# Performance work log

Hardware: AMD Instinct MI355X
Metric: run time of the kernel (lower is better)

Reference implementation:

```python
import jax, jax.numpy as jnp
import numpy as np

B, L, H, T_MAX, D_ID, D_SZ, D_POS = 64, 1024, 256, 128, 128, 64, 128
V_ID, V_SZ = 65536, 256


def setup_inputs() -> dict:
    key = jax.random.key(0)
    ks = jax.random.split(key, 16)
    s = 0.02
    inp = {
        'obj_id': jax.random.randint(ks[0], (B,), 0, V_ID, dtype=jnp.int32),
        'obj_size': jax.random.randint(ks[1], (B,), 0, V_SZ, dtype=jnp.int32),
        'cache_lines': jax.random.randint(ks[2], (B, L), 0, V_ID, dtype=jnp.int32),
        'lengths': jax.random.randint(ks[3], (B,), 0, L, dtype=jnp.int32),
        'c0': jax.random.normal(ks[4], (B, H), jnp.float32),
        'h0': jax.random.normal(ks[5], (B, H), jnp.float32),
        'history': jax.random.normal(ks[6], (B, T_MAX - 1, H), jnp.float32),
        # learned parameters
        'obj_id_table': jax.random.normal(ks[7], (V_ID, D_ID), jnp.float32) * s,
        'obj_size_table': jax.random.normal(ks[8], (V_SZ, D_SZ), jnp.float32) * s,
        'pos_table': jax.random.normal(ks[9], (T_MAX, D_POS), jnp.float32) * s,
        'W_ih': jax.random.normal(ks[10], (4 * H, D_ID + D_SZ), jnp.float32) * s,
        'W_hh': jax.random.normal(ks[11], (4 * H, H), jnp.float32) * s,
        'b_ih': jnp.zeros((4 * H,), jnp.float32),
        'b_hh': jnp.zeros((4 * H,), jnp.float32),
        'attn_W': jax.random.normal(ks[12], (D_ID, H), jnp.float32) * s,
        'scorer_W': jax.random.normal(ks[13], (1, H + D_POS), jnp.float32) * s,
        'scorer_b': jnp.zeros((1,), jnp.float32),
        'reuse_W': jax.random.normal(ks[14], (1, H + D_POS), jnp.float32) * s,
        'reuse_b': jnp.zeros((1,), jnp.float32),
    }
    return inp


def reference(obj_id, obj_size, cache_lines, lengths, c0, h0, history,
              obj_id_table, obj_size_table, pos_table,
              W_ih, W_hh, b_ih, b_hh, attn_W,
              scorer_W, scorer_b, reuse_W, reuse_b):
    # --- embed current access and run one LSTMCell step ---
    x = jnp.concatenate([obj_id_table[obj_id], obj_size_table[obj_size]], axis=-1)  # (B, D_ID+D_SZ)
    gates = x @ W_ih.T + b_ih + h0 @ W_hh.T + b_hh  # (B, 4H)
    i, f, g, o = jnp.split(gates, 4, axis=-1)
    c = jax.nn.sigmoid(f) * c0 + jax.nn.sigmoid(i) * jnp.tanh(g)
    h = jax.nn.sigmoid(o) * jnp.tanh(c)

    # --- growing hidden-state history (deque bounded at max_attention_history) ---
    hist = jnp.concatenate([history, h[:, None, :]], axis=1)  # (B, T, H)
    T = hist.shape[1]
    pos = jnp.broadcast_to(pos_table[:T][None], (hist.shape[0], T, pos_table.shape[1]))
    values = jnp.concatenate([hist, pos], axis=-1)  # (B, T, H+P)

    # --- cache line embeddings (cache_lines_embedder == obj_id_embedder) ---
    q = obj_id_table[cache_lines]  # (B, L, D_ID)

    # --- General (bilinear) multi-query attention over history ---
    scores = jnp.einsum('bld,dh,bth->blt', q, attn_W, hist)  # (B, L, T)
    weights = jax.nn.softmax(scores, axis=-1)
    contexts = jnp.einsum('blt,btv->blv', weights, values)  # (B, L, H+P)

    # --- heads ---
    line_scores = jax.nn.softmax((contexts @ scorer_W.T + scorer_b)[..., 0], axis=-1)  # (B, L)
    pred_reuse = (contexts @ reuse_W.T + reuse_b)[..., 0]  # (B, L)

    # --- mask_renormalize over valid (unpadded) cache lines ---
    valid = jnp.maximum(lengths, 1)[:, None]  # min_len=1 in pad()
    mask = (jnp.arange(line_scores.shape[1])[None, :] < valid).astype(line_scores.dtype)
    masked = line_scores * mask
    denom = masked.sum(axis=-1, keepdims=True)
    probs = masked / jnp.where(denom > 0, denom, 1.0)
    return probs, pred_reuse
```

## Files before the change

kernel.cpp:

```cpp
#include <hip/hip_runtime.h>
#include <math.h>

#define BB 64
#define LL 1024
#define HH 256
#define TT 128
#define D_ID 128
#define D_SZ 64
#define D_POS 128
#define DX 192

typedef short s16x8 __attribute__((ext_vector_type(8)));
typedef float f32x16 __attribute__((ext_vector_type(16)));
typedef unsigned short u16x8 __attribute__((ext_vector_type(8)));

__device__ __forceinline__ unsigned short f2bf(float f) {
    unsigned u = __float_as_uint(f);
    unsigned r = u + 0x7fffu + ((u >> 16) & 1u);
    return (unsigned short)(r >> 16);
}

__device__ __forceinline__ s16x8 pack8(float4 a, float4 b) {
    u16x8 p;
    p[0] = f2bf(a.x); p[1] = f2bf(a.y); p[2] = f2bf(a.z); p[3] = f2bf(a.w);
    p[4] = f2bf(b.x); p[5] = f2bf(b.y); p[6] = f2bf(b.z); p[7] = f2bf(b.w);
    return (s16x8)p;
}

__global__ void embed_kernel(const int* __restrict__ obj_id,
                             const int* __restrict__ obj_size,
                             const float* __restrict__ h0,
                             const float* __restrict__ obj_id_table,
                             const float* __restrict__ obj_size_table,
                             float* __restrict__ xh_t) {
    int tid = threadIdx.x;
    int b = tid & 63;
    int k = blockIdx.x * 4 + (tid >> 6);
    float v;
    if (k < D_ID)      v = obj_id_table[(size_t)obj_id[b] * D_ID + k];
    else if (k < DX)   v = obj_size_table[(size_t)obj_size[b] * D_SZ + (k - D_ID)];
    else               v = h0[b * HH + (k - DX)];
    xh_t[k * 64 + b] = v;
}

__global__ void gates_kernel(const float* __restrict__ xh_t,
                             const float* __restrict__ W_ih,
                             const float* __restrict__ W_hh,
                             const float* __restrict__ b_ih,
                             const float* __restrict__ b_hh,
                             const float* __restrict__ c0,
                             float* __restrict__ h_new) {
    int j = blockIdx.x;
    int tid = threadIdx.x;
    int b = tid & 63;
    int q = __builtin_amdgcn_readfirstlane(tid >> 6);
    int r = q * HH + j;
    __shared__ float gS[256];

    float acc = b_ih[r] + b_hh[r];
    const float* wi = W_ih + (size_t)r * DX;
    const float* wh = W_hh + (size_t)r * HH;
#pragma unroll 16
    for (int k = 0; k < DX; ++k)
        acc += wi[k] * xh_t[k * 64 + b];
#pragma unroll 16
    for (int k = 0; k < HH; ++k)
        acc += wh[k] * xh_t[(DX + k) * 64 + b];
    gS[q * 64 + b] = acc;
    __syncthreads();

    if (tid < 64) {
        float ig = 1.f / (1.f + expf(-gS[tid]));
        float fg = 1.f / (1.f + expf(-gS[64 + tid]));
        float gg = tanhf(gS[128 + tid]);
        float og = 1.f / (1.f + expf(-gS[192 + tid]));
        float c = fg * c0[tid * HH + j] + ig * gg;
        h_new[tid * HH + j] = og * tanhf(c);
    }
}

__global__ void proj_kernel(const float* __restrict__ history,
                            const float* __restrict__ h_new,
                            const float* __restrict__ attn_W,
                            const float* __restrict__ pos_table,
                            const float* __restrict__ scorer_W,
                            const float* __restrict__ reuse_W,
                            unsigned short* __restrict__ hp,
                            float* __restrict__ sv,
                            float* __restrict__ rv) {
    int blk = blockIdx.x;
    int tid = threadIdx.x;

    if (blk >= BB * 16) {
        int idx = blk - BB * 16;
        int b = idx >> 2;
        int which = (idx >> 1) & 1;
        int t = (idx & 1) * 64 + tid;
        const float* w = which ? reuse_W : scorer_W;
        const float* hrow = (t < TT - 1)
            ? history + ((size_t)b * (TT - 1) + t) * HH
            : h_new + (size_t)b * HH;
        float acc = 0.f;
#pragma unroll 8
        for (int k = 0; k < HH / 4; ++k) {
            float4 hv = *(const float4*)(hrow + 4 * k);
            float4 wv = *(const float4*)(w + 4 * k);
            acc += hv.x * wv.x + hv.y * wv.y + hv.z * wv.z + hv.w * wv.w;
        }
        const float* prow = pos_table + (size_t)t * D_POS;
#pragma unroll 8
        for (int k = 0; k < D_POS / 4; ++k) {
            float4 pv = *(const float4*)(prow + 4 * k);
            float4 wv = *(const float4*)(w + HH + 4 * k);
            acc += pv.x * wv.x + pv.y * wv.y + pv.z * wv.z + pv.w * wv.w;
        }
        (which ? rv : sv)[b * TT + t] = acc;
        return;
    }

    int b  = blk >> 4;
    int t0 = ((blk >> 2) & 3) * 32;
    int d0 = (blk & 3) * 32;
    int lane = tid;
    int ln = lane & 31, half = lane >> 5;

    int t = t0 + ln;
    const float* arow = (t < TT - 1)
        ? history + ((size_t)b * (TT - 1) + t) * HH
        : h_new + (size_t)b * HH;
    const float* brow = attn_W + (size_t)(d0 + ln) * HH;

    f32x16 acc;
#pragma unroll
    for (int r = 0; r < 16; ++r) acc[r] = 0.f;

#pragma unroll
    for (int ks = 0; ks < 16; ++ks) {
        int off = ks * 16 + half * 8;
        float4 a0 = *(const float4*)(arow + off);
        float4 a1 = *(const float4*)(arow + off + 4);
        float4 b0 = *(const float4*)(brow + off);
        float4 b1 = *(const float4*)(brow + off + 4);
        acc = __builtin_amdgcn_mfma_f32_32x32x16_bf16(
            pack8(a0, a1), pack8(b0, b1), acc, 0, 0, 0);
    }

#pragma unroll
    for (int r = 0; r < 16; ++r) {
        int tt = t0 + (r & 3) + 8 * (r >> 2) + 4 * half;
        hp[((size_t)b * TT + tt) * D_ID + d0 + ln] = f2bf(acc[r]);
    }
}

__global__ void attn_kernel(const int* __restrict__ cache_lines,
                            const float* __restrict__ obj_id_table,
                            const unsigned short* __restrict__ hp,
                            const float* __restrict__ sv,
                            const float* __restrict__ rv,
                            const float* __restrict__ scorer_b,
                            const float* __restrict__ reuse_b,
                            float* __restrict__ logits,
                            float* __restrict__ out_reuse) {
    int b  = blockIdx.x >> 3;
    int l0 = (blockIdx.x & 7) * 128;
    int tid = threadIdx.x;
    __shared__ unsigned short qS[16384];
    __shared__ unsigned short hpS[16384];

    {
        int l = tid & 127;
        int cl = cache_lines[b * LL + l0 + l];
        const float* qrow = obj_id_table + (size_t)cl * D_ID;
        int lhi = (l >> 5) * 8, llo = l & 31;
#pragma unroll
        for (int i = 0; i < 8; ++i) {
            int u = 2 * i + (tid >> 7);
            float4 f0 = *(const float4*)(qrow + u * 8);
            float4 f1 = *(const float4*)(qrow + u * 8 + 4);
            *(s16x8*)(qS + (((lhi + (u >> 1)) * 64) + (u & 1) * 32 + llo) * 8) =
                pack8(f0, f1);
        }
    }
    {
        int t = tid & 127;
        const unsigned short* hrow = hp + ((size_t)b * TT + t) * D_ID;
        int thi = t >> 5, tlo = t & 31;
#pragma unroll
        for (int i = 0; i < 8; ++i) {
            int u = 2 * i + (tid >> 7);
            u16x8 p = *(const u16x8*)(hrow + u * 8);
            *(u16x8*)(hpS + ((((u >> 1) * 4 + thi) * 64) + (u & 1) * 32 + tlo) * 8) = p;
        }
    }
    __syncthreads();

    int w = tid >> 6;
    int lane = tid & 63;
    int ln = lane & 31, half = lane >> 5;

    f32x16 acc[4];
#pragma unroll
    for (int tt = 0; tt < 4; ++tt)
#pragma unroll
        for (int r = 0; r < 16; ++r) acc[tt][r] = 0.f;

    const unsigned short* qw = qS + w * 8 * 512;
#pragma unroll
    for (int k = 0; k < 8; ++k) {
        s16x8 a = *(const s16x8*)(qw + k * 512 + lane * 8);
#pragma unroll
        for (int tt = 0; tt < 4; ++tt) {
            s16x8 bf = *(const s16x8*)(hpS + (k * 4 + tt) * 512 + lane * 8);
            acc[tt] = __builtin_amdgcn_mfma_f32_32x32x16_bf16(a, bf, acc[tt], 0, 0, 0);
        }
    }

    float sv_r[4], rv_r[4];
#pragma unroll
    for (int tt = 0; tt < 4; ++tt) {
        sv_r[tt] = sv[b * TT + tt * 32 + ln];
        rv_r[tt] = rv[b * TT + tt * 32 + ln];
    }
    float sb = scorer_b[0], rb = reuse_b[0];

#pragma unroll
    for (int r = 0; r < 16; ++r) {
        float v0 = acc[0][r], v1 = acc[1][r], v2 = acc[2][r], v3 = acc[3][r];
        float m = fmaxf(fmaxf(v0, v1), fmaxf(v2, v3));
#pragma unroll
        for (int off = 1; off < 32; off <<= 1) m = fmaxf(m, __shfl_xor(m, off));
        float e0 = __expf(v0 - m), e1 = __expf(v1 - m),
              e2 = __expf(v2 - m), e3 = __expf(v3 - m);
        float s  = e0 + e1 + e2 + e3;
        float lg = e0 * sv_r[0] + e1 * sv_r[1] + e2 * sv_r[2] + e3 * sv_r[3];
        float rg = e0 * rv_r[0] + e1 * rv_r[1] + e2 * rv_r[2] + e3 * rv_r[3];
#pragma unroll
        for (int off = 1; off < 32; off <<= 1) {
            s  += __shfl_xor(s, off);
            lg += __shfl_xor(lg, off);
            rg += __shfl_xor(rg, off);
        }
        if (ln == 0) {
            int row = (r & 3) + 8 * (r >> 2) + 4 * half;
            int l = l0 + w * 32 + row;
            logits[b * LL + l] = lg / s + sb;
            out_reuse[b * LL + l] = rg / s + rb;
        }
    }
}

__global__ void finalsm_kernel(const float* __restrict__ logits,
                               const int* __restrict__ lengths,
                               float* __restrict__ out_probs) {
    int b = blockIdx.x;
    int tid = threadIdx.x;
    int valid = max(lengths[b], 1);
    float v[4];
    float m = -1e30f;
#pragma unroll
    for (int i = 0; i < 4; ++i) {
        int l = tid + 256 * i;
        v[i] = (l < valid) ? logits[b * LL + l] : -1e30f;
        m = fmaxf(m, v[i]);
    }
#pragma unroll
    for (int off = 1; off < 64; off <<= 1) m = fmaxf(m, __shfl_xor(m, off));
    __shared__ float redm[4];
    __shared__ float reds[4];
    int wave = tid >> 6;
    if ((tid & 63) == 0) redm[wave] = m;
    __syncthreads();
    m = fmaxf(fmaxf(redm[0], redm[1]), fmaxf(redm[2], redm[3]));
    float e[4];
    float s = 0.f;
#pragma unroll
    for (int i = 0; i < 4; ++i) {
        int l = tid + 256 * i;
        e[i] = (l < valid) ? expf(v[i] - m) : 0.f;
        s += e[i];
    }
#pragma unroll
    for (int off = 1; off < 64; off <<= 1) s += __shfl_xor(s, off);
    if ((tid & 63) == 0) reds[wave] = s;
    __syncthreads();
    s = reds[0] + reds[1] + reds[2] + reds[3];
    float inv = 1.f / s;
#pragma unroll
    for (int i = 0; i < 4; ++i)
        out_probs[b * LL + tid + 256 * i] = e[i] * inv;
}

extern "C" void kernel_launch(void* const* d_in, const int* in_sizes, int n_in,
                              void* d_out, int out_size, void* d_ws, size_t ws_size,
                              hipStream_t stream) {
    const int*   obj_id         = (const int*)d_in[0];
    const int*   obj_size       = (const int*)d_in[1];
    const int*   cache_lines    = (const int*)d_in[2];
    const int*   lengths        = (const int*)d_in[3];
    const float* c0             = (const float*)d_in[4];
    const float* h0             = (const float*)d_in[5];
    const float* history        = (const float*)d_in[6];
    const float* obj_id_table   = (const float*)d_in[7];
    const float* obj_size_table = (const float*)d_in[8];
    const float* pos_table      = (const float*)d_in[9];
    const float* W_ih           = (const float*)d_in[10];
    const float* W_hh           = (const float*)d_in[11];
    const float* b_ih           = (const float*)d_in[12];
    const float* b_hh           = (const float*)d_in[13];
    const float* attn_W         = (const float*)d_in[14];
    const float* scorer_W       = (const float*)d_in[15];
    const float* scorer_b       = (const float*)d_in[16];
    const float* reuse_W        = (const float*)d_in[17];
    const float* reuse_b        = (const float*)d_in[18];

    float* out = (float*)d_out;
    float* out_probs = out;
    float* out_reuse = out + BB * LL;

    char* ws = (char*)d_ws;
    float*          h_new  = (float*)(ws);
    unsigned short* hp     = (unsigned short*)(ws + 65536);
    float*          sv     = (float*)(ws + 65536 + 2097152);
    float*          rv     = (float*)(ws + 65536 + 2097152 + 32768);
    float*          xh_t   = (float*)(ws + 65536 + 2097152 + 65536);
    float*          logits = (float*)(ws + 65536 + 2097152 + 65536);

    hipLaunchKernelGGL(embed_kernel, dim3(112), dim3(256), 0, stream,
                       obj_id, obj_size, h0, obj_id_table, obj_size_table, xh_t);
    hipLaunchKernelGGL(gates_kernel, dim3(HH), dim3(256), 0, stream,
                       xh_t, W_ih, W_hh, b_ih, b_hh, c0, h_new);
    hipLaunchKernelGGL(proj_kernel, dim3(BB * 16 + BB * 4), dim3(64), 0, stream,
                       history, h_new, attn_W, pos_table, scorer_W, reuse_W,
                       hp, sv, rv);
    hipLaunchKernelGGL(attn_kernel, dim3(BB * 8), dim3(256), 0, stream,
                       cache_lines, obj_id_table, hp, sv, rv,
                       scorer_b, reuse_b, logits, out_reuse);
    hipLaunchKernelGGL(finalsm_kernel, dim3(BB), dim3(256), 0, stream,
                       logits, lengths, out_probs);
}
```

Before: 160.7 us.

## Fuse embed into gates, recompute history projection inside attention blocks

Folds the embedding gather into the gates kernel through shared memory, and moves the sv/rv head dot products for history rows into extra blocks of the gates launch. The bilinear projection of history through attn_W is recomputed per attention block with MFMA straight into shared memory, which removes the hp workspace round trip. The last timestep's head values are computed in-block from h_new. This cuts five launches to three, but each of the 8 blocks per batch redundantly recomputes the 128x128x256 projection.

```diff
diff --git a/kernel.cpp b/kernel.cpp
--- a/kernel.cpp
+++ b/kernel.cpp
@@ -13,6 +13,7 @@
 typedef short s16x8 __attribute__((ext_vector_type(8)));
 typedef float f32x16 __attribute__((ext_vector_type(16)));
 typedef unsigned short u16x8 __attribute__((ext_vector_type(8)));
+typedef unsigned short u16x4 __attribute__((ext_vector_type(4)));
 
 __device__ __forceinline__ unsigned short f2bf(float f) {
     unsigned u = __float_as_uint(f);
@@ -27,45 +28,122 @@
     return (s16x8)p;
 }
 
-__global__ void embed_kernel(const int* __restrict__ obj_id,
+__global__ void gates_kernel(const int* __restrict__ obj_id,
                              const int* __restrict__ obj_size,
                              const float* __restrict__ h0,
+                             const float* __restrict__ c0,
                              const float* __restrict__ obj_id_table,
                              const float* __restrict__ obj_size_table,
-                             float* __restrict__ xh_t) {
-    int tid = threadIdx.x;
-    int b = tid & 63;
-    int k = blockIdx.x * 4 + (tid >> 6);
-    float v;
-    if (k < D_ID)      v = obj_id_table[(size_t)obj_id[b] * D_ID + k];
-    else if (k < DX)   v = obj_size_table[(size_t)obj_size[b] * D_SZ + (k - D_ID)];
-    else               v = h0[b * HH + (k - DX)];
-    xh_t[k * 64 + b] = v;
-}
-
-__global__ void gates_kernel(const float* __restrict__ xh_t,
+                             const float* __restrict__ history,
+                             const float* __restrict__ pos_table,
                              const float* __restrict__ W_ih,
                              const float* __restrict__ W_hh,
                              const float* __restrict__ b_ih,
                              const float* __restrict__ b_hh,
-                             const float* __restrict__ c0,
-                             float* __restrict__ h_new) {
+                             const float* __restrict__ scorer_W,
+                             const float* __restrict__ reuse_W,
+                             float* __restrict__ h_new,
+                             float* __restrict__ sv,
+                             float* __restrict__ rv) {
+    int tid = threadIdx.x;
+
+    if (blockIdx.x >= HH) {
+        int b = blockIdx.x - HH;
+        int which = tid >> 7;
+        int t = tid & 127;
+        if (t == TT - 1) return;
+        const float* w = which ? reuse_W : scorer_W;
+        const float* hrow = history + ((size_t)b * (TT - 1) + t) * HH;
+        float acc = 0.f;
+#pragma unroll 8
+        for (int k = 0; k < HH / 4; ++k) {
+            float4 hv = *(const float4*)(hrow + 4 * k);
+            float4 wv = *(const float4*)(w + 4 * k);
+            acc += hv.x * wv.x + hv.y * wv.y + hv.z * wv.z + hv.w * wv.w;
+        }
+        const float* prow = pos_table + (size_t)t * D_POS;
+#pragma unroll 8
+        for (int k = 0; k < D_POS / 4; ++k) {
+            float4 pv = *(const float4*)(prow + 4 * k);
+            float4 wv = *(const float4*)(w + HH + 4 * k);
+            acc += pv.x * wv.x + pv.y * wv.y + pv.z * wv.z + pv.w * wv.w;
+        }
+        (which ? rv : sv)[b * TT + t] = acc;
+        return;
+    }
+
+    __shared__ float xhS[224 * 64];
+    __shared__ float gS[256];
+
     int j = blockIdx.x;
-    int tid = threadIdx.x;
     int b = tid & 63;
     int q = __builtin_amdgcn_readfirstlane(tid >> 6);
     int r = q * HH + j;
-    __shared__ float gS[256];
-
-    float acc = b_ih[r] + b_hh[r];
     const float* wi = W_ih + (size_t)r * DX;
     const float* wh = W_hh + (size_t)r * HH;
+    float acc = b_ih[r] + b_hh[r];
+
+    int sb = tid >> 2;
+    int c4 = tid & 3;
+
+    {
+        const float* row = obj_id_table + (size_t)obj_id[sb] * D_ID;
+#pragma unroll
+        for (int i = 0; i < 8; ++i) {
+            int k = c4 * 4 + i * 16;
+            float4 v = *(const float4*)(row + k);
+            xhS[(k + 0) * 64 + sb] = v.x;
+            xhS[(k + 1) * 64 + sb] = v.y;
+            xhS[(k + 2) * 64 + sb] = v.z;
+            xhS[(k + 3) * 64 + sb] = v.w;
+        }
+        const float* srow = obj_size_table + (size_t)obj_size[sb] * D_SZ;
+#pragma unroll
+        for (int i = 0; i < 4; ++i) {
+            int k = c4 * 4 + i * 16;
+            float4 v = *(const float4*)(srow + k);
+            xhS[(D_ID + k + 0) * 64 + sb] = v.x;
+            xhS[(D_ID + k + 1) * 64 + sb] = v.y;
+            xhS[(D_ID + k + 2) * 64 + sb] = v.z;
+            xhS[(D_ID + k + 3) * 64 + sb] = v.w;
+        }
+        const float* h0row = h0 + (size_t)sb * HH;
+#pragma unroll
+        for (int i = 0; i < 2; ++i) {
+            int k = c4 * 4 + i * 16;
+            float4 v = *(const float4*)(h0row + k);
+            xhS[(DX + k + 0) * 64 + sb] = v.x;
+            xhS[(DX + k + 1) * 64 + sb] = v.y;
+            xhS[(DX + k + 2) * 64 + sb] = v.z;
+            xhS[(DX + k + 3) * 64 + sb] = v.w;
+        }
+    }
+    __syncthreads();
 #pragma unroll 16
     for (int k = 0; k < DX; ++k)
-        acc += wi[k] * xh_t[k * 64 + b];
+        acc += wi[k] * xhS[k * 64 + b];
+#pragma unroll 8
+    for (int k = 0; k < 32; ++k)
+        acc += wh[k] * xhS[(DX + k) * 64 + b];
+    __syncthreads();
+
+    {
+        const float* h0row = h0 + (size_t)sb * HH + 32;
+#pragma unroll
+        for (int i = 0; i < 14; ++i) {
+            int k = c4 * 4 + i * 16;
+            float4 v = *(const float4*)(h0row + k);
+            xhS[(k + 0) * 64 + sb] = v.x;
+            xhS[(k + 1) * 64 + sb] = v.y;
+            xhS[(k + 2) * 64 + sb] = v.z;
+            xhS[(k + 3) * 64 + sb] = v.w;
+        }
+    }
+    __syncthreads();
 #pragma unroll 16
-    for (int k = 0; k < HH; ++k)
-        acc += wh[k] * xh_t[(DX + k) * 64 + b];
+    for (int k = 0; k < 224; ++k)
+        acc += wh[32 + k] * xhS[k * 64 + b];
+
     gS[q * 64 + b] = acc;
     __syncthreads();
 
@@ -79,84 +157,16 @@
     }
 }
 
-__global__ void proj_kernel(const float* __restrict__ history,
+__global__ void attn_kernel(const int* __restrict__ cache_lines,
+                            const float* __restrict__ obj_id_table,
+                            const float* __restrict__ history,
                             const float* __restrict__ h_new,
                             const float* __restrict__ attn_W,
                             const float* __restrict__ pos_table,
+                            const float* __restrict__ sv,
+                            const float* __restrict__ rv,
                             const float* __restrict__ scorer_W,
                             const float* __restrict__ reuse_W,
-                            unsigned short* __restrict__ hp,
-                            float* __restrict__ sv,
-                            float* __restrict__ rv) {
-    int blk = blockIdx.x;
-    int tid = threadIdx.x;
-
-    if (blk >= BB * 16) {
-        int idx = blk - BB * 16;
-        int b = idx >> 2;
-        int which = (idx >> 1) & 1;
-        int t = (idx & 1) * 64 + tid;
-        const float* w = which ? reuse_W : scorer_W;
-        const float* hrow = (t < TT - 1)
-            ? history + ((size_t)b * (TT - 1) + t) * HH
-            : h_new + (size_t)b * HH;
-        float acc = 0.f;
-#pragma unroll 8
-        for (int k = 0; k < HH / 4; ++k) {
-            float4 hv = *(const float4*)(hrow + 4 * k);
-            float4 wv = *(const float4*)(w + 4 * k);
-            acc += hv.x * wv.x + hv.y * wv.y + hv.z * wv.z + hv.w * wv.w;
-        }
-        const float* prow = pos_table + (size_t)t * D_POS;
-#pragma unroll 8
-        for (int k = 0; k < D_POS / 4; ++k) {
-            float4 pv = *(const float4*)(prow + 4 * k);
-            float4 wv = *(const float4*)(w + HH + 4 * k);
-            acc += pv.x * wv.x + pv.y * wv.y + pv.z * wv.z + pv.w * wv.w;
-        }
-        (which ? rv : sv)[b * TT + t] = acc;
-        return;
-    }
-
-    int b  = blk >> 4;
-    int t0 = ((blk >> 2) & 3) * 32;
-    int d0 = (blk & 3) * 32;
-    int lane = tid;
-    int ln = lane & 31, half = lane >> 5;
-
-    int t = t0 + ln;
-    const float* arow = (t < TT - 1)
-        ? history + ((size_t)b * (TT - 1) + t) * HH
-        : h_new + (size_t)b * HH;
-    const float* brow = attn_W + (size_t)(d0 + ln) * HH;
-
-    f32x16 acc;
-#pragma unroll
-    for (int r = 0; r < 16; ++r) acc[r] = 0.f;
-
-#pragma unroll
-    for (int ks = 0; ks < 16; ++ks) {
-        int off = ks * 16 + half * 8;
-        float4 a0 = *(const float4*)(arow + off);
-        float4 a1 = *(const float4*)(arow + off + 4);
-        float4 b0 = *(const float4*)(brow + off);
-        float4 b1 = *(const float4*)(brow + off + 4);
-        acc = __builtin_amdgcn_mfma_f32_32x32x16_bf16(
-            pack8(a0, a1), pack8(b0, b1), acc, 0, 0, 0);
-    }
-
-#pragma unroll
-    for (int r = 0; r < 16; ++r) {
-        int tt = t0 + (r & 3) + 8 * (r >> 2) + 4 * half;
-        hp[((size_t)b * TT + tt) * D_ID + d0 + ln] = f2bf(acc[r]);
-    }
-}
-
-__global__ void attn_kernel(const int* __restrict__ cache_lines,
-                            const float* __restrict__ obj_id_table,
-                            const unsigned short* __restrict__ hp,
-                            const float* __restrict__ sv,
-                            const float* __restrict__ rv,
                             const float* __restrict__ scorer_b,
                             const float* __restrict__ reuse_b,
                             float* __restrict__ logits,
@@ -166,6 +176,11 @@
     int tid = threadIdx.x;
     __shared__ unsigned short qS[16384];
     __shared__ unsigned short hpS[16384];
+    __shared__ float s127[2];
+
+    int w = tid >> 6;
+    int lane = tid & 63;
+    int ln = lane & 31, half = lane >> 5;
 
     {
         int l = tid & 127;
@@ -181,28 +196,73 @@
                 pack8(f0, f1);
         }
     }
+
     {
-        int t = tid & 127;
-        const unsigned short* hrow = hp + ((size_t)b * TT + t) * D_ID;
-        int thi = t >> 5, tlo = t & 31;
-#pragma unroll
-        for (int i = 0; i < 8; ++i) {
-            int u = 2 * i + (tid >> 7);
-            u16x8 p = *(const u16x8*)(hrow + u * 8);
-            *(u16x8*)(hpS + ((((u >> 1) * 4 + thi) * 64) + (u & 1) * 32 + tlo) * 8) = p;
-        }
-    }
-    __syncthreads();
-
-    int w = tid >> 6;
-    int lane = tid & 63;
-    int ln = lane & 31, half = lane >> 5;
+        const float* arow = attn_W + (size_t)(32 * w + ln) * HH;
+        const float* brow[4];
+#pragma unroll
+        for (int tt = 0; tt < 4; ++tt) {
+            int t = tt * 32 + ln;
+            brow[tt] = (t < TT - 1) ? history + ((size_t)b * (TT - 1) + t) * HH
+                                    : h_new + (size_t)b * HH;
+        }
+        f32x16 pacc[4];
+#pragma unroll
+        for (int tt = 0; tt < 4; ++tt)
+#pragma unroll
+            for (int rr = 0; rr < 16; ++rr) pacc[tt][rr] = 0.f;
+
+#pragma unroll 4
+        for (int ks = 0; ks < 16; ++ks) {
+            int off = ks * 16 + half * 8;
+            float4 a0 = *(const float4*)(arow + off);
+            float4 a1 = *(const float4*)(arow + off + 4);
+            s16x8 af = pack8(a0, a1);
+#pragma unroll
+            for (int tt = 0; tt < 4; ++tt) {
+                float4 b0 = *(const float4*)(brow[tt] + off);
+                float4 b1 = *(const float4*)(brow[tt] + off + 4);
+                pacc[tt] = __builtin_amdgcn_mfma_f32_32x32x16_bf16(
+                    af, pack8(b0, b1), pacc[tt], 0, 0, 0);
+            }
+        }
+#pragma unroll
+        for (int tt = 0; tt < 4; ++tt)
+#pragma unroll
+            for (int qd = 0; qd < 4; ++qd) {
+                u16x4 v;
+                v[0] = f2bf(pacc[tt][4 * qd + 0]);
+                v[1] = f2bf(pacc[tt][4 * qd + 1]);
+                v[2] = f2bf(pacc[tt][4 * qd + 2]);
+                v[3] = f2bf(pacc[tt][4 * qd + 3]);
+                int sa = ((2 * w + (qd >> 1)) * 4 + tt) * 512 +
+                         (qd & 1) * 256 + ln * 8 + 4 * half;
+                *(u16x4*)(hpS + sa) = v;
+            }
+    }
+
+    if (w < 2) {
+        const float* wv = w ? reuse_W : scorer_W;
+        float a = 0.f;
+#pragma unroll
+        for (int i = 0; i < 6; ++i) {
+            int idx = lane + 64 * i;
+            float x = (idx < HH)
+                ? h_new[(size_t)b * HH + idx]
+                : pos_table[(size_t)(TT - 1) * D_POS + (idx - HH)];
+            a += wv[idx] * x;
+        }
+#pragma unroll
+        for (int off = 1; off < 64; off <<= 1) a += __shfl_xor(a, off);
+        if (lane == 0) s127[w] = a;
+    }
+    __syncthreads();
 
     f32x16 acc[4];
 #pragma unroll
     for (int tt = 0; tt < 4; ++tt)
 #pragma unroll
-        for (int r = 0; r < 16; ++r) acc[tt][r] = 0.f;
+        for (int rr = 0; rr < 16; ++rr) acc[tt][rr] = 0.f;
 
     const unsigned short* qw = qS + w * 8 * 512;
 #pragma unroll
@@ -221,6 +281,7 @@
         sv_r[tt] = sv[b * TT + tt * 32 + ln];
         rv_r[tt] = rv[b * TT + tt * 32 + ln];
     }
+    if (ln == 31) { sv_r[3] = s127[0]; rv_r[3] = s127[1]; }
     float sb = scorer_b[0], rb = reuse_b[0];
 
 #pragma unroll
@@ -318,22 +379,18 @@
     float* out_reuse = out + BB * LL;
 
     char* ws = (char*)d_ws;
-    float*          h_new  = (float*)(ws);
-    unsigned short* hp     = (unsigned short*)(ws + 65536);
-    float*          sv     = (float*)(ws + 65536 + 2097152);
-    float*          rv     = (float*)(ws + 65536 + 2097152 + 32768);
-    float*          xh_t   = (float*)(ws + 65536 + 2097152 + 65536);
-    float*          logits = (float*)(ws + 65536 + 2097152 + 65536);
-
-    hipLaunchKernelGGL(embed_kernel, dim3(112), dim3(256), 0, stream,
-                       obj_id, obj_size, h0, obj_id_table, obj_size_table, xh_t);
-    hipLaunchKernelGGL(gates_kernel, dim3(HH), dim3(256), 0, stream,
-                       xh_t, W_ih, W_hh, b_ih, b_hh, c0, h_new);
-    hipLaunchKernelGGL(proj_kernel, dim3(BB * 16 + BB * 4), dim3(64), 0, stream,
-                       history, h_new, attn_W, pos_table, scorer_W, reuse_W,
-                       hp, sv, rv);
+    float* h_new  = (float*)(ws);
+    float* sv     = (float*)(ws + 65536);
+    float* rv     = (float*)(ws + 98304);
+    float* logits = (float*)(ws + 131072);
+
+    hipLaunchKernelGGL(gates_kernel, dim3(HH + BB), dim3(256), 0, stream,
+                       obj_id, obj_size, h0, c0, obj_id_table, obj_size_table,
+                       history, pos_table, W_ih, W_hh, b_ih, b_hh,
+                       scorer_W, reuse_W, h_new, sv, rv);
     hipLaunchKernelGGL(attn_kernel, dim3(BB * 8), dim3(256), 0, stream,
-                       cache_lines, obj_id_table, hp, sv, rv,
+                       cache_lines, obj_id_table, history, h_new, attn_W,
+                       pos_table, sv, rv, scorer_W, reuse_W,
                        scorer_b, reuse_b, logits, out_reuse);
     hipLaunchKernelGGL(finalsm_kernel, dim3(BB), dim3(256), 0, stream,
                        logits, lengths, out_probs);
```

Result: slower. 193.0 us (+20.0%).

## Split attention into single-wave blocks loading operands directly from global memory

Applied to the files above, without the earlier changes.

The attention kernel now launches one 64-thread wave per block, each handling 32 cache lines, instead of 256-thread blocks staging query and projected history tiles through shared memory. Query rows are gathered into registers and packed to bf16 directly. History fragments are read from global/L2 for each MFMA, which removes the shared-memory staging and the barrier and raises block count for latency hiding. The cost is that each wave re-reads the per-batch history tile from cache rather than sharing it within a block.

```diff
diff --git a/kernel.cpp b/kernel.cpp
--- a/kernel.cpp
+++ b/kernel.cpp
@@ -152,67 +152,28 @@
     }
 }
 
-__global__ void attn_kernel(const int* __restrict__ cache_lines,
-                            const float* __restrict__ obj_id_table,
-                            const unsigned short* __restrict__ hp,
-                            const float* __restrict__ sv,
-                            const float* __restrict__ rv,
-                            const float* __restrict__ scorer_b,
-                            const float* __restrict__ reuse_b,
-                            float* __restrict__ logits,
-                            float* __restrict__ out_reuse) {
-    int b  = blockIdx.x >> 3;
-    int l0 = (blockIdx.x & 7) * 128;
-    int tid = threadIdx.x;
-    __shared__ unsigned short qS[16384];
-    __shared__ unsigned short hpS[16384];
-
-    {
-        int l = tid & 127;
-        int cl = cache_lines[b * LL + l0 + l];
-        const float* qrow = obj_id_table + (size_t)cl * D_ID;
-        int lhi = (l >> 5) * 8, llo = l & 31;
-#pragma unroll
-        for (int i = 0; i < 8; ++i) {
-            int u = 2 * i + (tid >> 7);
-            float4 f0 = *(const float4*)(qrow + u * 8);
-            float4 f1 = *(const float4*)(qrow + u * 8 + 4);
-            *(s16x8*)(qS + (((lhi + (u >> 1)) * 64) + (u & 1) * 32 + llo) * 8) =
-                pack8(f0, f1);
-        }
-    }
-    {
-        int t = tid & 127;
-        const unsigned short* hrow = hp + ((size_t)b * TT + t) * D_ID;
-        int thi = t >> 5, tlo = t & 31;
-#pragma unroll
-        for (int i = 0; i < 8; ++i) {
-            int u = 2 * i + (tid >> 7);
-            u16x8 p = *(const u16x8*)(hrow + u * 8);
-            *(u16x8*)(hpS + ((((u >> 1) * 4 + thi) * 64) + (u & 1) * 32 + tlo) * 8) = p;
-        }
-    }
-    __syncthreads();
-
-    int w = tid >> 6;
-    int lane = tid & 63;
+__global__ void __launch_bounds__(64, 2)
+attn_kernel(const int* __restrict__ cache_lines,
+            const float* __restrict__ obj_id_table,
+            const unsigned short* __restrict__ hp,
+            const float* __restrict__ sv,
+            const float* __restrict__ rv,
+            const float* __restrict__ scorer_b,
+            const float* __restrict__ reuse_b,
+            float* __restrict__ logits,
+            float* __restrict__ out_reuse) {
+    int b  = blockIdx.x >> 5;
+    int l0 = (blockIdx.x & 31) * 32;
+    int lane = threadIdx.x;
     int ln = lane & 31, half = lane >> 5;
 
-    f32x16 acc[4];
-#pragma unroll
-    for (int tt = 0; tt < 4; ++tt)
-#pragma unroll
-        for (int r = 0; r < 16; ++r) acc[tt][r] = 0.f;
-
-    const unsigned short* qw = qS + w * 8 * 512;
-#pragma unroll
-    for (int k = 0; k < 8; ++k) {
-        s16x8 a = *(const s16x8*)(qw + k * 512 + lane * 8);
-#pragma unroll
-        for (int tt = 0; tt < 4; ++tt) {
-            s16x8 bf = *(const s16x8*)(hpS + (k * 4 + tt) * 512 + lane * 8);
-            acc[tt] = __builtin_amdgcn_mfma_f32_32x32x16_bf16(a, bf, acc[tt], 0, 0, 0);
-        }
+    int cl = cache_lines[b * LL + l0 + ln];
+    const float* qrow = obj_id_table + (size_t)cl * D_ID + half * 8;
+    float4 qa[8], qb[8];
+#pragma unroll
+    for (int ks = 0; ks < 8; ++ks) {
+        qa[ks] = *(const float4*)(qrow + ks * 16);
+        qb[ks] = *(const float4*)(qrow + ks * 16 + 4);
     }
 
     float sv_r[4], rv_r[4];
@@ -222,6 +183,26 @@
         rv_r[tt] = rv[b * TT + tt * 32 + ln];
     }
     float sb = scorer_b[0], rb = reuse_b[0];
+
+    s16x8 qf[8];
+#pragma unroll
+    for (int ks = 0; ks < 8; ++ks) qf[ks] = pack8(qa[ks], qb[ks]);
+
+    const unsigned short* hpb = hp + (size_t)b * TT * D_ID + half * 8;
+    f32x16 acc[4];
+#pragma unroll
+    for (int tt = 0; tt < 4; ++tt)
+#pragma unroll
+        for (int r = 0; r < 16; ++r) acc[tt][r] = 0.f;
+
+#pragma unroll
+    for (int k = 0; k < 8; ++k) {
+#pragma unroll
+        for (int tt = 0; tt < 4; ++tt) {
+            s16x8 bf = *(const s16x8*)(hpb + (size_t)(tt * 32 + ln) * D_ID + k * 16);
+            acc[tt] = __builtin_amdgcn_mfma_f32_32x32x16_bf16(qf[k], bf, acc[tt], 0, 0, 0);
+        }
+    }
 
 #pragma unroll
     for (int r = 0; r < 16; ++r) {
@@ -242,7 +223,7 @@
         }
         if (ln == 0) {
             int row = (r & 3) + 8 * (r >> 2) + 4 * half;
-            int l = l0 + w * 32 + row;
+            int l = l0 + row;
             logits[b * LL + l] = lg / s + sb;
             out_reuse[b * LL + l] = rg / s + rb;
         }
@@ -332,7 +313,7 @@
     hipLaunchKernelGGL(proj_kernel, dim3(BB * 16 + BB * 4), dim3(64), 0, stream,
                        history, h_new, attn_W, pos_table, scorer_W, reuse_W,
                        hp, sv, rv);
-    hipLaunchKernelGGL(attn_kernel, dim3(BB * 8), dim3(256), 0, stream,
+    hipLaunchKernelGGL(attn_kernel, dim3(BB * 32), dim3(64), 0, stream,
                        cache_lines, obj_id_table, hp, sv, rv,
                        scorer_b, reuse_b, logits, out_reuse);
     hipLaunchKernelGGL(finalsm_kernel, dim3(BB), dim3(256), 0, stream,
```

Result: slower. 165.3 us (+2.8%).
